# Performance work log

Measured on AMD Instinct MI355X. Metric: run time of the kernel, lower is better.

Reference implementation:

```python
import jax, jax.numpy as jnp
import numpy as np

B1, B2, CHUNK, HID, T = 64, 16, 128, 64, 131072
N_CHUNKS = 128


def setup_inputs() -> dict:
    key = jax.random.key(0)
    ks = jax.random.split(key, 12)
    # positive prices so log(p) is finite
    p = jax.random.uniform(ks[0], (T, 2), jnp.float32) * 2.0 + 0.5
    inds = jax.random.randint(ks[1], (B1,), 0, 100000, dtype=jnp.int32)
    open_slices = jax.random.randint(ks[2], (B1, B2, 1), 0, T, dtype=jnp.int32)
    ls_probs = jax.random.uniform(ks[3], (B1, B2, 1, 1), jnp.float32)
    open_probs = jax.random.uniform(ks[4], (B1, B2, 1, 1), jnp.float32)
    open_hx = jax.random.normal(ks[5], (B1, B2, 2, HID), jnp.float32) * 0.1
    s = 1.0 / np.sqrt(HID)
    # torch nn.LSTM params: gate order i,f,g,o
    W_ih = jax.random.uniform(ks[6], (4 * HID, 2), jnp.float32, -s, s)
    W_hh = jax.random.uniform(ks[7], (4 * HID, HID), jnp.float32, -s, s)
    b_ih = jax.random.uniform(ks[8], (4 * HID,), jnp.float32, -s, s)
    b_hh = jax.random.uniform(ks[9], (4 * HID,), jnp.float32, -s, s)
    W_out = jax.random.uniform(ks[10], (1, HID), jnp.float32, -s, s)
    b_out = jax.random.uniform(ks[11], (1,), jnp.float32, -s, s)
    return {"inds": inds, "p": p, "ls_probs": ls_probs, "open_probs": open_probs,
            "open_slices": open_slices, "open_hx": open_hx,
            "W_ih": W_ih, "W_hh": W_hh, "b_ih": b_ih, "b_hh": b_hh,
            "W_out": W_out, "b_out": b_out, "n_chunks": N_CHUNKS}


def reference(inds, p, ls_probs, open_probs, open_slices, open_hx,
              W_ih, W_hh, b_ih, b_hh, W_out, b_out, n_chunks):
    b1, b2 = open_hx.shape[:2]
    hid = open_hx.shape[-1]
    C = CHUNK
    h0 = open_hx[:, :, 0, :].reshape(b1 * b2, hid)
    c0 = open_hx[:, :, 1, :].reshape(b1 * b2, hid)
    open_logp = jnp.log(p[open_slices])  # (b1, b2, 1, 2)
    # sliding-window gather base: idx[i,j,t] = inds[i] + j + t (per-chunk offset added in scan)
    base = (inds[:, None, None]
            + jnp.arange(b2, dtype=inds.dtype)[None, :, None]
            + jnp.arange(C, dtype=inds.dtype)[None, None, :])  # (b1, b2, C)
    bias = b_ih + b_hh

    def lstm_chunk(x, h, c):  # x: (N, C, 2)
        xg = x @ W_ih.T + bias  # precompute input projection: (N, C, 4H)
        def step(carry, xg_t):
            h, c = carry
            g = xg_t + h @ W_hh.T
            i, f, gg, o = jnp.split(g, 4, axis=-1)
            c = jax.nn.sigmoid(f) * c + jax.nn.sigmoid(i) * jnp.tanh(gg)
            h = jax.nn.sigmoid(o) * jnp.tanh(c)
            return (h, c), h
        (h, c), hs = jax.lax.scan(step, (h, c), xg.swapaxes(0, 1))
        return hs.swapaxes(0, 1), h, c  # (N, C, H)

    def chunk_step(carry, offset):
        h, c, last_nd, loss = carry
        idx = base + offset * C                      # (b1, b2, C)
        p_chunk = p[idx]                             # (b1, b2, C, 2)
        x = p_chunk - p_chunk[:, :, :1, :]           # re-center on first step of chunk
        out, h, c = lstm_chunk(x.reshape(b1 * b2, C, 2), h, c)
        probs = jax.nn.sigmoid(out.reshape(b1, b2, C, hid) @ W_out.T + b_out)  # (b1,b2,C,1)
        not_done = last_nd * jnp.cumprod(1.0 - probs[:, :, :-1], axis=2)       # (b1,b2,C-1,1)
        probs = jnp.concatenate([probs[:, :, :1], probs[:, :, 1:] * not_done], axis=2)
        last_nd = not_done[:, :, -1:, :]
        logp = jnp.log(p_chunk)
        payoff = ls_probs * (logp - open_logp) + (1.0 - ls_probs) * (open_logp - logp)
        loss = loss + jnp.sum(open_probs * probs * payoff)
        return (h, c, last_nd, loss), None

    init = (h0, c0, jnp.ones((b1, b2, 1, 1), p.dtype), jnp.zeros((), p.dtype))
    (_, _, _, loss), _ = jax.lax.scan(chunk_step, init, jnp.arange(n_chunks))
    return loss
```

## Files before the change

### kernel.cpp

```cpp
#include <hip/hip_runtime.h>


#define CH  128
#define HID 64

typedef __fp16 f16x2 __attribute__((ext_vector_type(2)));

__device__ __forceinline__ float rlf(float v, int l) {
  return __builtin_bit_cast(float, __builtin_amdgcn_readlane(__builtin_bit_cast(int, v), l));
}
__device__ __forceinline__ int rli(int v, int l) { return __builtin_amdgcn_readlane(v, l); }
__device__ __forceinline__ int packh(float a, float b) {
  return __builtin_bit_cast(int, __builtin_amdgcn_cvt_pkrtz(a, b));
}
__device__ __forceinline__ f16x2 h2(int v) { return __builtin_bit_cast(f16x2, v); }
__device__ __forceinline__ float frcp(float x) { return __builtin_amdgcn_rcpf(x); }
__device__ __forceinline__ float sigm(float x) { return frcp(1.0f + __expf(-x)); }
__device__ __forceinline__ float tanh_(float x) {
  float e = __expf(2.0f * x);
  return 1.0f - 2.0f * frcp(e + 1.0f);
}
template <int CTRL, int RMASK>
__device__ __forceinline__ float dpp_add(float v) {
  int x = __builtin_amdgcn_update_dpp(0, __builtin_bit_cast(int, v), CTRL, RMASK, 0xF, true);
  return v + __builtin_bit_cast(float, x);
}
__device__ __forceinline__ float dpp_xor1(float v) {
  int x = __builtin_amdgcn_update_dpp(0, __builtin_bit_cast(int, v), 0xB1, 0xF, 0xF, true);
  return __builtin_bit_cast(float, x);
}
__device__ __forceinline__ float dpp_wave_sum(float v) {
  v = dpp_add<0x111, 0xF>(v);
  v = dpp_add<0x112, 0xF>(v);
  v = dpp_add<0x114, 0xF>(v);
  v = dpp_add<0x118, 0xF>(v);
  v = dpp_add<0x142, 0xA>(v);
  v = dpp_add<0x143, 0xC>(v);
  return v;
}

__global__ __attribute__((amdgpu_flat_work_group_size(128, 128), amdgpu_waves_per_eu(2, 2)))
void pc_lstm_kernel(const int* __restrict__ inds,
                    const float* __restrict__ p,
                    const float* __restrict__ ls_probs,
                    const float* __restrict__ open_probs,
                    const int* __restrict__ open_slices,
                    const float* __restrict__ open_hx,
                    const float* __restrict__ W_ih,
                    const float* __restrict__ W_hh,
                    const float* __restrict__ b_ih,
                    const float* __restrict__ b_hh,
                    const float* __restrict__ W_out,
                    const float* __restrict__ b_out,
                    const int* __restrict__ n_chunks_p,
                    float* __restrict__ out)
{
  __shared__ __fp16 ring[2][CH][HID];
  __shared__ int prod;
  __shared__ int cons;

  const int tid  = threadIdx.x;
  const int wv   = tid >> 6;
  const int lane = tid & 63;
  const int s    = blockIdx.x;
  const int n_chunks = n_chunks_p[0];
  const int tbase = inds[s >> 4] + (s & 15);
  const float2* p2 = (const float2*)p;

  if (tid == 0) { prod = 0; cons = 0; }
  __syncthreads();

  if (wv == 0) {
    int W0[HID / 2], W1[HID / 2], W2[HID / 2], W3[HID / 2];
    {
      const float2* r0 = (const float2*)(W_hh + (0 * HID + lane) * HID);
      const float2* r1 = (const float2*)(W_hh + (1 * HID + lane) * HID);
      const float2* r2 = (const float2*)(W_hh + (2 * HID + lane) * HID);
      const float2* r3 = (const float2*)(W_hh + (3 * HID + lane) * HID);
#pragma unroll
      for (int j = 0; j < HID / 2; ++j) {
        float2 v0 = r0[j], v1 = r1[j], v2 = r2[j], v3 = r3[j];
        W0[j] = packh(v0.x, v0.y);
        W1[j] = packh(v1.x, v1.y);
        W2[j] = packh(v2.x, v2.y);
        W3[j] = packh(v3.x, v3.y);
      }
    }
    float wxa[4], wxb[4], bb[4];
#pragma unroll
    for (int g = 0; g < 4; ++g) {
      const int r = g * HID + lane;
      wxa[g] = W_ih[2 * r];
      wxb[g] = W_ih[2 * r + 1];
      bb[g]  = b_ih[r] + b_hh[r];
    }
    float h = open_hx[(s * 2 + 0) * HID + lane];
    float c = open_hx[(s * 2 + 1) * HID + lane];

    float2 curA = p2[tbase + lane];
    float2 curB = p2[tbase + HID + lane];
    float2 nxtA = curA, nxtB = curB;

    for (int off = 0; off < n_chunks; ++off) {
      if (off) { curA = nxtA; curB = nxtB; }
      const float px0 = rlf(curA.x, 0);
      const float px1 = rlf(curA.y, 0);
      float2 xA, xB;
      xA.x = curA.x - px0; xA.y = curA.y - px1;
      xB.x = curB.x - px0; xB.y = curB.y - px1;
      if (off + 1 < n_chunks) {
        const int nb = tbase + (off + 1) * CH;
        nxtA = p2[nb + lane];
        nxtB = p2[nb + HID + lane];
      }
      while (__hip_atomic_load(&cons, __ATOMIC_ACQUIRE, __HIP_MEMORY_SCOPE_WORKGROUP) + 2 <= off)
        __builtin_amdgcn_s_sleep(8);

      __fp16* slot = &ring[off & 1][0][0];
#pragma unroll
      for (int hf = 0; hf < 2; ++hf) {
        const float xcx = hf ? xB.x : xA.x;
        const float xcy = hf ? xB.y : xA.y;
#pragma unroll 1
        for (int tl = 0; tl < 64; ++tl) {
          const int hp = packh(h, dpp_xor1(h));
          const float x0 = rlf(xcx, tl);
          const float x1 = rlf(xcy, tl);

          float A0 = bb[0], A1 = bb[1], A2 = bb[2], A3 = bb[3];
          float B0 = fmaf(x1, wxb[0], x0 * wxa[0]);
          float B1 = fmaf(x1, wxb[1], x0 * wxa[1]);
          float B2 = fmaf(x1, wxb[2], x0 * wxa[2]);
          float B3 = fmaf(x1, wxb[3], x0 * wxa[3]);
#pragma unroll
          for (int j = 0; j < 16; ++j) {
            const f16x2 ha = h2(rli(hp, 2 * j));
            const f16x2 hb = h2(rli(hp, 2 * j + 32));
            A0 = __builtin_amdgcn_fdot2(ha, h2(W0[j]),      A0, false);
            B0 = __builtin_amdgcn_fdot2(hb, h2(W0[j + 16]), B0, false);
            A1 = __builtin_amdgcn_fdot2(ha, h2(W1[j]),      A1, false);
            B1 = __builtin_amdgcn_fdot2(hb, h2(W1[j + 16]), B1, false);
            A2 = __builtin_amdgcn_fdot2(ha, h2(W2[j]),      A2, false);
            B2 = __builtin_amdgcn_fdot2(hb, h2(W2[j + 16]), B2, false);
            A3 = __builtin_amdgcn_fdot2(ha, h2(W3[j]),      A3, false);
            B3 = __builtin_amdgcn_fdot2(hb, h2(W3[j + 16]), B3, false);
          }
          const float ig = sigm(A0 + B0);
          const float fg = sigm(A1 + B1);
          const float gg = tanh_(A2 + B2);
          const float og = sigm(A3 + B3);
          c = fmaf(fg, c, ig * gg);
          h = og * tanh_(c);

          slot[(hf * 64 + tl) * HID + lane] = (__fp16)h;
        }
      }
      if (lane == 0)
        __hip_atomic_store(&prod, off + 1, __ATOMIC_RELEASE, __HIP_MEMORY_SCOPE_WORKGROUP);
    }
  } else {
    const float wo   = W_out[lane];
    const float bout = b_out[0];
    const int   os   = open_slices[s];
    const float OL   = __logf(p[2 * os]) + __logf(p[2 * os + 1]);
    const float coef = open_probs[s] * (2.0f * ls_probs[s] - 1.0f);

    float S = 1.0f, D = 1.0f, lsum = 0.0f, psum = 0.0f;

    for (int off = 0; off < n_chunks; ++off) {
      const int cb = tbase + off * CH;
      const float2 cA = p2[cb + lane];
      const float2 cB = p2[cb + HID + lane];
      const float LA = __logf(cA.x) + __logf(cA.y);
      const float LB = __logf(cB.x) + __logf(cB.y);

      while (__hip_atomic_load(&prod, __ATOMIC_ACQUIRE, __HIP_MEMORY_SCOPE_WORKGROUP) <= off)
        __builtin_amdgcn_s_sleep(32);

      const __fp16* slot = &ring[off & 1][0][0];
#pragma unroll 1
      for (int tt = 0; tt < CH; ++tt) {
        const float hv = (float)slot[tt * HID + lane];
        const float z  = rlf(dpp_wave_sum(hv * wo), 63);
        const float pr = sigm(z + bout);
        const float Lt = (tt < 64) ? rlf(LA, tt) : rlf(LB, tt - 64);
        const float pn = (tt == 0) ? pr : pr * D;
        lsum = fmaf(pn, Lt, lsum);
        psum += pn;
        if (tt == 0)           D = S * (1.0f - pr);
        else if (tt < CH - 1)  D *= (1.0f - pr);
        else                   S = D;
      }
      if (lane == 0)
        __hip_atomic_store(&cons, off + 1, __ATOMIC_RELEASE, __HIP_MEMORY_SCOPE_WORKGROUP);
    }
    if (lane == 0) atomicAdd(out, coef * (lsum - OL * psum));
  }
}

extern "C" void kernel_launch(void* const* d_in, const int* in_sizes, int n_in,
                              void* d_out, int out_size, void* d_ws, size_t ws_size,
                              hipStream_t stream) {
  (void)hipMemsetAsync(d_out, 0, sizeof(float), stream);

  pc_lstm_kernel<<<dim3(1024), dim3(128), 0, stream>>>(
      (const int*)d_in[0],
      (const float*)d_in[1],
      (const float*)d_in[2],
      (const float*)d_in[3],
      (const int*)d_in[4],
      (const float*)d_in[5],
      (const float*)d_in[6],
      (const float*)d_in[7],
      (const float*)d_in[8],
      (const float*)d_in[9],
      (const float*)d_in[10],
      (const float*)d_in[11],
      (const int*)d_in[12],
      (float*)d_out);
}
```

Baseline: 8.087 ms.

## Split recurrent matvec across both waves with per-step barrier handoff

Both waves now hold half of W_hh in registers. Wave 1 computes the partial dot product for the second half of h and passes it to wave 0 through LDS, in lockstep with two __syncthreads per timestep. This is meant to halve the serial fdot2 and readlane chain on the critical path. The loss computation on wave 1 is delayed by one chunk and interleaved into the same loop, replacing the atomic producer/consumer flags, and the waves_per_eu attribute is swapped for plain launch bounds. The cost is barrier and LDS round-trip latency added to every recurrent step.

```diff
diff --git a/kernel.cpp b/kernel.cpp
--- a/kernel.cpp
+++ b/kernel.cpp
@@ -39,7 +39,7 @@
   return v;
 }
 
-__global__ __attribute__((amdgpu_flat_work_group_size(128, 128), amdgpu_waves_per_eu(2, 2)))
+__global__ __launch_bounds__(128)
 void pc_lstm_kernel(const int* __restrict__ inds,
                     const float* __restrict__ p,
                     const float* __restrict__ ls_probs,
@@ -56,8 +56,8 @@
                     float* __restrict__ out)
 {
   __shared__ __fp16 ring[2][CH][HID];
-  __shared__ int prod;
-  __shared__ int cons;
+  __shared__ int    hpbuf[16];
+  __shared__ float  pbuf[64][4];
 
   const int tid  = threadIdx.x;
   const int wv   = tid >> 6;
@@ -67,26 +67,33 @@
   const int tbase = inds[s >> 4] + (s & 15);
   const float2* p2 = (const float2*)p;
 
-  if (tid == 0) { prod = 0; cons = 0; }
-  __syncthreads();
+  int W0[16], W1[16], W2[16], W3[16];
+  {
+    const int kb = wv * 32;
+    const float2* r0 = (const float2*)(W_hh + (0 * HID + lane) * HID + kb);
+    const float2* r1 = (const float2*)(W_hh + (1 * HID + lane) * HID + kb);
+    const float2* r2 = (const float2*)(W_hh + (2 * HID + lane) * HID + kb);
+    const float2* r3 = (const float2*)(W_hh + (3 * HID + lane) * HID + kb);
+#pragma unroll
+    for (int j = 0; j < 16; ++j) {
+      float2 v0 = r0[j], v1 = r1[j], v2 = r2[j], v3 = r3[j];
+      W0[j] = packh(v0.x, v0.y);
+      W1[j] = packh(v1.x, v1.y);
+      W2[j] = packh(v2.x, v2.y);
+      W3[j] = packh(v3.x, v3.y);
+    }
+  }
+
+  float wxa[4], wxb[4], bb[4];
+  float h = 0.0f, c = 0.0f;
+  int   hp = 0;
+  float2 nxtA, nxtB, xA, xB;
+  float wo = 0.0f, bout = 0.0f, OL = 0.0f, coef = 0.0f;
+  float S = 1.0f, D = 1.0f, lsum = 0.0f, psum = 0.0f;
+  float2 lagA, lagB;
+  float lagLA = 0.0f, lagLB = 0.0f;
 
   if (wv == 0) {
-    int W0[HID / 2], W1[HID / 2], W2[HID / 2], W3[HID / 2];
-    {
-      const float2* r0 = (const float2*)(W_hh + (0 * HID + lane) * HID);
-      const float2* r1 = (const float2*)(W_hh + (1 * HID + lane) * HID);
-      const float2* r2 = (const float2*)(W_hh + (2 * HID + lane) * HID);
-      const float2* r3 = (const float2*)(W_hh + (3 * HID + lane) * HID);
-#pragma unroll
-      for (int j = 0; j < HID / 2; ++j) {
-        float2 v0 = r0[j], v1 = r1[j], v2 = r2[j], v3 = r3[j];
-        W0[j] = packh(v0.x, v0.y);
-        W1[j] = packh(v1.x, v1.y);
-        W2[j] = packh(v2.x, v2.y);
-        W3[j] = packh(v3.x, v3.y);
-      }
-    }
-    float wxa[4], wxb[4], bb[4];
 #pragma unroll
     for (int g = 0; g < 4; ++g) {
       const int r = g * HID + lane;
@@ -94,18 +101,26 @@
       wxb[g] = W_ih[2 * r + 1];
       bb[g]  = b_ih[r] + b_hh[r];
     }
-    float h = open_hx[(s * 2 + 0) * HID + lane];
-    float c = open_hx[(s * 2 + 1) * HID + lane];
-
-    float2 curA = p2[tbase + lane];
-    float2 curB = p2[tbase + HID + lane];
-    float2 nxtA = curA, nxtB = curB;
-
-    for (int off = 0; off < n_chunks; ++off) {
-      if (off) { curA = nxtA; curB = nxtB; }
+    h = open_hx[(s * 2 + 0) * HID + lane];
+    c = open_hx[(s * 2 + 1) * HID + lane];
+    hp = packh(h, dpp_xor1(h));
+    if (lane >= 32 && !(lane & 1)) hpbuf[(lane - 32) >> 1] = hp;
+    nxtA = p2[tbase + lane];
+    nxtB = p2[tbase + HID + lane];
+  } else {
+    wo   = W_out[lane];
+    bout = b_out[0];
+    const int os = open_slices[s];
+    OL   = __logf(p[2 * os]) + __logf(p[2 * os + 1]);
+    coef = open_probs[s] * (2.0f * ls_probs[s] - 1.0f);
+  }
+  __syncthreads();
+
+  for (int off = 0; off < n_chunks; ++off) {
+    if (wv == 0) {
+      const float2 curA = nxtA, curB = nxtB;
       const float px0 = rlf(curA.x, 0);
       const float px1 = rlf(curA.y, 0);
-      float2 xA, xB;
       xA.x = curA.x - px0; xA.y = curA.y - px1;
       xB.x = curB.x - px0; xB.y = curB.y - px1;
       if (off + 1 < n_chunks) {
@@ -113,86 +128,102 @@
         nxtA = p2[nb + lane];
         nxtB = p2[nb + HID + lane];
       }
-      while (__hip_atomic_load(&cons, __ATOMIC_ACQUIRE, __HIP_MEMORY_SCOPE_WORKGROUP) + 2 <= off)
-        __builtin_amdgcn_s_sleep(8);
-
-      __fp16* slot = &ring[off & 1][0][0];
-#pragma unroll
-      for (int hf = 0; hf < 2; ++hf) {
-        const float xcx = hf ? xB.x : xA.x;
-        const float xcy = hf ? xB.y : xA.y;
+    } else {
+      if (off) {
+        lagLA = __logf(lagA.x) + __logf(lagA.y);
+        lagLB = __logf(lagB.x) + __logf(lagB.y);
+      }
+      const int lb = tbase + off * CH;
+      lagA = p2[lb + lane];
+      lagB = p2[lb + HID + lane];
+    }
+    const int doloss = (off > 0);
+    const int rpar = off & 1;
+
+#pragma unroll
+    for (int hf = 0; hf < 2; ++hf) {
 #pragma unroll 1
-        for (int tl = 0; tl < 64; ++tl) {
-          const int hp = packh(h, dpp_xor1(h));
-          const float x0 = rlf(xcx, tl);
-          const float x1 = rlf(xcy, tl);
-
-          float A0 = bb[0], A1 = bb[1], A2 = bb[2], A3 = bb[3];
-          float B0 = fmaf(x1, wxb[0], x0 * wxa[0]);
-          float B1 = fmaf(x1, wxb[1], x0 * wxa[1]);
-          float B2 = fmaf(x1, wxb[2], x0 * wxa[2]);
-          float B3 = fmaf(x1, wxb[3], x0 * wxa[3]);
+      for (int tl = 0; tl < 64; ++tl) {
+        const int tt = (hf << 6) + tl;
+        float A0, A1, A2, A3;
+        float hv = 0.0f;
+
+        if (wv == 0) {
+          const float x0 = rlf(hf ? xB.x : xA.x, tl);
+          const float x1 = rlf(hf ? xB.y : xA.y, tl);
+          A0 = fmaf(x1, wxb[0], fmaf(x0, wxa[0], bb[0]));
+          A1 = fmaf(x1, wxb[1], fmaf(x0, wxa[1], bb[1]));
+          A2 = fmaf(x1, wxb[2], fmaf(x0, wxa[2], bb[2]));
+          A3 = fmaf(x1, wxb[3], fmaf(x0, wxa[3], bb[3]));
 #pragma unroll
           for (int j = 0; j < 16; ++j) {
             const f16x2 ha = h2(rli(hp, 2 * j));
-            const f16x2 hb = h2(rli(hp, 2 * j + 32));
-            A0 = __builtin_amdgcn_fdot2(ha, h2(W0[j]),      A0, false);
-            B0 = __builtin_amdgcn_fdot2(hb, h2(W0[j + 16]), B0, false);
-            A1 = __builtin_amdgcn_fdot2(ha, h2(W1[j]),      A1, false);
-            B1 = __builtin_amdgcn_fdot2(hb, h2(W1[j + 16]), B1, false);
-            A2 = __builtin_amdgcn_fdot2(ha, h2(W2[j]),      A2, false);
-            B2 = __builtin_amdgcn_fdot2(hb, h2(W2[j + 16]), B2, false);
-            A3 = __builtin_amdgcn_fdot2(ha, h2(W3[j]),      A3, false);
-            B3 = __builtin_amdgcn_fdot2(hb, h2(W3[j + 16]), B3, false);
+            A0 = __builtin_amdgcn_fdot2(ha, h2(W0[j]), A0, false);
+            A1 = __builtin_amdgcn_fdot2(ha, h2(W1[j]), A1, false);
+            A2 = __builtin_amdgcn_fdot2(ha, h2(W2[j]), A2, false);
+            A3 = __builtin_amdgcn_fdot2(ha, h2(W3[j]), A3, false);
           }
-          const float ig = sigm(A0 + B0);
-          const float fg = sigm(A1 + B1);
-          const float gg = tanh_(A2 + B2);
-          const float og = sigm(A3 + B3);
+        } else {
+          const int hw = hpbuf[lane & 15];
+          if (doloss) hv = (float)ring[rpar ^ 1][tt][lane];
+          float P0 = 0.f, P1 = 0.f, P2 = 0.f, P3 = 0.f;
+#pragma unroll
+          for (int j = 0; j < 16; ++j) {
+            const f16x2 hb = h2(rli(hw, j));
+            P0 = __builtin_amdgcn_fdot2(hb, h2(W0[j]), P0, false);
+            P1 = __builtin_amdgcn_fdot2(hb, h2(W1[j]), P1, false);
+            P2 = __builtin_amdgcn_fdot2(hb, h2(W2[j]), P2, false);
+            P3 = __builtin_amdgcn_fdot2(hb, h2(W3[j]), P3, false);
+          }
+          pbuf[lane][0] = P0; pbuf[lane][1] = P1;
+          pbuf[lane][2] = P2; pbuf[lane][3] = P3;
+          A0 = A1 = A2 = A3 = 0.0f;
+        }
+        __syncthreads();
+
+        if (wv == 0) {
+          const float4 P = *(const float4*)&pbuf[lane][0];
+          const float ig = sigm(A0 + P.x);
+          const float fg = sigm(A1 + P.y);
+          const float gg = tanh_(A2 + P.z);
+          const float og = sigm(A3 + P.w);
           c = fmaf(fg, c, ig * gg);
           h = og * tanh_(c);
-
-          slot[(hf * 64 + tl) * HID + lane] = (__fp16)h;
+          hp = packh(h, dpp_xor1(h));
+          if (lane >= 32 && !(lane & 1)) hpbuf[(lane - 32) >> 1] = hp;
+          ring[rpar][tt][lane] = (__fp16)h;
+        } else if (doloss) {
+          const float z  = rlf(dpp_wave_sum(hv * wo), 63);
+          const float pr = sigm(z + bout);
+          const float Lt = hf ? rlf(lagLB, tl) : rlf(lagLA, tl);
+          const float pn = (tt == 0) ? pr : pr * D;
+          lsum = fmaf(pn, Lt, lsum);
+          psum += pn;
+          if (tt == 0)           D = S * (1.0f - pr);
+          else if (tt < CH - 1)  D *= (1.0f - pr);
+          else                   S = D;
         }
+        __syncthreads();
       }
-      if (lane == 0)
-        __hip_atomic_store(&prod, off + 1, __ATOMIC_RELEASE, __HIP_MEMORY_SCOPE_WORKGROUP);
-    }
-  } else {
-    const float wo   = W_out[lane];
-    const float bout = b_out[0];
-    const int   os   = open_slices[s];
-    const float OL   = __logf(p[2 * os]) + __logf(p[2 * os + 1]);
-    const float coef = open_probs[s] * (2.0f * ls_probs[s] - 1.0f);
-
-    float S = 1.0f, D = 1.0f, lsum = 0.0f, psum = 0.0f;
-
-    for (int off = 0; off < n_chunks; ++off) {
-      const int cb = tbase + off * CH;
-      const float2 cA = p2[cb + lane];
-      const float2 cB = p2[cb + HID + lane];
-      const float LA = __logf(cA.x) + __logf(cA.y);
-      const float LB = __logf(cB.x) + __logf(cB.y);
-
-      while (__hip_atomic_load(&prod, __ATOMIC_ACQUIRE, __HIP_MEMORY_SCOPE_WORKGROUP) <= off)
-        __builtin_amdgcn_s_sleep(32);
-
-      const __fp16* slot = &ring[off & 1][0][0];
+    }
+  }
+
+  if (wv == 1) {
+    lagLA = __logf(lagA.x) + __logf(lagA.y);
+    lagLB = __logf(lagB.x) + __logf(lagB.y);
+    const int rpar = (n_chunks - 1) & 1;
 #pragma unroll 1
-      for (int tt = 0; tt < CH; ++tt) {
-        const float hv = (float)slot[tt * HID + lane];
-        const float z  = rlf(dpp_wave_sum(hv * wo), 63);
-        const float pr = sigm(z + bout);
-        const float Lt = (tt < 64) ? rlf(LA, tt) : rlf(LB, tt - 64);
-        const float pn = (tt == 0) ? pr : pr * D;
-        lsum = fmaf(pn, Lt, lsum);
-        psum += pn;
-        if (tt == 0)           D = S * (1.0f - pr);
-        else if (tt < CH - 1)  D *= (1.0f - pr);
-        else                   S = D;
-      }
-      if (lane == 0)
-        __hip_atomic_store(&cons, off + 1, __ATOMIC_RELEASE, __HIP_MEMORY_SCOPE_WORKGROUP);
+    for (int tt = 0; tt < CH; ++tt) {
+      const float hv = (float)ring[rpar][tt][lane];
+      const float z  = rlf(dpp_wave_sum(hv * wo), 63);
+      const float pr = sigm(z + bout);
+      const float Lt = (tt < 64) ? rlf(lagLA, tt) : rlf(lagLB, tt - 64);
+      const float pn = (tt == 0) ? pr : pr * D;
+      lsum = fmaf(pn, Lt, lsum);
+      psum += pn;
+      if (tt == 0)           D = S * (1.0f - pr);
+      else if (tt < CH - 1)  D *= (1.0f - pr);
+      else                   S = D;
     }
     if (lane == 0) atomicAdd(out, coef * (lsum - OL * psum));
   }
```

Result: slower. 10.72 ms (+32.5%).

## Stream packed fp16 W_hh from global memory each step instead of holding it in registers

Applied to the files above, without the earlier changes.

Adds a staging kernel that packs W_hh into fp16 pairs laid out as int4 per lane and gate. The recurrent loop now loads these weights from global memory (L1/L2 cached) on every timestep instead of keeping 128 VGPRs of weights resident. This frees registers, but it puts 32 vector memory loads per step on the serial critical path of the LSTM recurrence, and their latency may dominate.

```diff
diff --git a/kernel.cpp b/kernel.cpp
--- a/kernel.cpp
+++ b/kernel.cpp
@@ -39,6 +39,18 @@
   return v;
 }
 
+__global__ void stage_w(const float* __restrict__ W_hh, int4* __restrict__ ws) {
+  const int lane = threadIdx.x;
+  const int j    = blockIdx.x;
+  const int k    = 2 * j;
+  int4 v;
+  v.x = packh(W_hh[(0 * HID + lane) * HID + k], W_hh[(0 * HID + lane) * HID + k + 1]);
+  v.y = packh(W_hh[(1 * HID + lane) * HID + k], W_hh[(1 * HID + lane) * HID + k + 1]);
+  v.z = packh(W_hh[(2 * HID + lane) * HID + k], W_hh[(2 * HID + lane) * HID + k + 1]);
+  v.w = packh(W_hh[(3 * HID + lane) * HID + k], W_hh[(3 * HID + lane) * HID + k + 1]);
+  ws[j * 64 + lane] = v;
+}
+
 __global__ __attribute__((amdgpu_flat_work_group_size(128, 128), amdgpu_waves_per_eu(2, 2)))
 void pc_lstm_kernel(const int* __restrict__ inds,
                     const float* __restrict__ p,
@@ -47,12 +59,12 @@
                     const int* __restrict__ open_slices,
                     const float* __restrict__ open_hx,
                     const float* __restrict__ W_ih,
-                    const float* __restrict__ W_hh,
                     const float* __restrict__ b_ih,
                     const float* __restrict__ b_hh,
                     const float* __restrict__ W_out,
                     const float* __restrict__ b_out,
                     const int* __restrict__ n_chunks_p,
+                    const int4* __restrict__ wpack,
                     float* __restrict__ out)
 {
   __shared__ __fp16 ring[2][CH][HID];
@@ -71,21 +83,6 @@
   __syncthreads();
 
   if (wv == 0) {
-    int W0[HID / 2], W1[HID / 2], W2[HID / 2], W3[HID / 2];
-    {
-      const float2* r0 = (const float2*)(W_hh + (0 * HID + lane) * HID);
-      const float2* r1 = (const float2*)(W_hh + (1 * HID + lane) * HID);
-      const float2* r2 = (const float2*)(W_hh + (2 * HID + lane) * HID);
-      const float2* r3 = (const float2*)(W_hh + (3 * HID + lane) * HID);
-#pragma unroll
-      for (int j = 0; j < HID / 2; ++j) {
-        float2 v0 = r0[j], v1 = r1[j], v2 = r2[j], v3 = r3[j];
-        W0[j] = packh(v0.x, v0.y);
-        W1[j] = packh(v1.x, v1.y);
-        W2[j] = packh(v2.x, v2.y);
-        W3[j] = packh(v3.x, v3.y);
-      }
-    }
     float wxa[4], wxb[4], bb[4];
 #pragma unroll
     for (int g = 0; g < 4; ++g) {
@@ -100,6 +97,8 @@
     float2 curA = p2[tbase + lane];
     float2 curB = p2[tbase + HID + lane];
     float2 nxtA = curA, nxtB = curB;
+
+    int woff = lane * (int)sizeof(int4);
 
     for (int off = 0; off < n_chunks; ++off) {
       if (off) { curA = nxtA; curB = nxtB; }
@@ -123,6 +122,9 @@
         const float xcy = hf ? xB.y : xA.y;
 #pragma unroll 1
         for (int tl = 0; tl < 64; ++tl) {
+          asm volatile("" : "+v"(woff));
+          const int4* wp = (const int4*)((const char*)wpack + woff);
+
           const int hp = packh(h, dpp_xor1(h));
           const float x0 = rlf(xcx, tl);
           const float x1 = rlf(xcy, tl);
@@ -134,16 +136,18 @@
           float B3 = fmaf(x1, wxb[3], x0 * wxa[3]);
 #pragma unroll
           for (int j = 0; j < 16; ++j) {
+            const int4 wa = wp[j * 64];
+            const int4 wb = wp[(j + 16) * 64];
             const f16x2 ha = h2(rli(hp, 2 * j));
             const f16x2 hb = h2(rli(hp, 2 * j + 32));
-            A0 = __builtin_amdgcn_fdot2(ha, h2(W0[j]),      A0, false);
-            B0 = __builtin_amdgcn_fdot2(hb, h2(W0[j + 16]), B0, false);
-            A1 = __builtin_amdgcn_fdot2(ha, h2(W1[j]),      A1, false);
-            B1 = __builtin_amdgcn_fdot2(hb, h2(W1[j + 16]), B1, false);
-            A2 = __builtin_amdgcn_fdot2(ha, h2(W2[j]),      A2, false);
-            B2 = __builtin_amdgcn_fdot2(hb, h2(W2[j + 16]), B2, false);
-            A3 = __builtin_amdgcn_fdot2(ha, h2(W3[j]),      A3, false);
-            B3 = __builtin_amdgcn_fdot2(hb, h2(W3[j + 16]), B3, false);
+            A0 = __builtin_amdgcn_fdot2(ha, h2(wa.x), A0, false);
+            B0 = __builtin_amdgcn_fdot2(hb, h2(wb.x), B0, false);
+            A1 = __builtin_amdgcn_fdot2(ha, h2(wa.y), A1, false);
+            B1 = __builtin_amdgcn_fdot2(hb, h2(wb.y), B1, false);
+            A2 = __builtin_amdgcn_fdot2(ha, h2(wa.z), A2, false);
+            B2 = __builtin_amdgcn_fdot2(hb, h2(wb.z), B2, false);
+            A3 = __builtin_amdgcn_fdot2(ha, h2(wa.w), A3, false);
+            B3 = __builtin_amdgcn_fdot2(hb, h2(wb.w), B3, false);
           }
           const float ig = sigm(A0 + B0);
           const float fg = sigm(A1 + B1);
@@ -203,6 +207,8 @@
                               hipStream_t stream) {
   (void)hipMemsetAsync(d_out, 0, sizeof(float), stream);
 
+  stage_w<<<dim3(32), dim3(64), 0, stream>>>((const float*)d_in[7], (int4*)d_ws);
+
   pc_lstm_kernel<<<dim3(1024), dim3(128), 0, stream>>>(
       (const int*)d_in[0],
       (const float*)d_in[1],
@@ -211,11 +217,11 @@
       (const int*)d_in[4],
       (const float*)d_in[5],
       (const float*)d_in[6],
-      (const float*)d_in[7],
       (const float*)d_in[8],
       (const float*)d_in[9],
       (const float*)d_in[10],
       (const float*)d_in[11],
       (const int*)d_in[12],
+      (const int4*)d_ws,
       (float*)d_out);
 }
```

New measurement: 18.66 ms. 131% more time.

## Compute LSTM recurrent matvec with MFMA 16x16x32 instead of fdot2 readlane loop

Applied to the files above, without the earlier changes.

Replaces the per-lane fdot2 loop, which broadcast h via 32 readlanes per step, with 32 MFMA 16x16x32 f16 ops per timestep. W_hh is held in registers as B fragments. h is spread into A fragments through ds_bpermute, and only row 0 of each output tile is used. The matvec wastes most of the MFMA rows, and each step now pays for ds_bpermute round-trips and MFMA latency on the serial recurrence. Launch bounds also change from the fixed waves_per_eu hint to __launch_bounds__(128).

```diff
diff --git a/kernel.cpp b/kernel.cpp
--- a/kernel.cpp
+++ b/kernel.cpp
@@ -4,16 +4,25 @@
 #define CH  128
 #define HID 64
 
-typedef __fp16 f16x2 __attribute__((ext_vector_type(2)));
+typedef __fp16 f16x8 __attribute__((ext_vector_type(8)));
+typedef float  f32x4 __attribute__((ext_vector_type(4)));
+typedef int    i32x4 __attribute__((ext_vector_type(4)));
+
+#define MFMA16(a, b, c) __builtin_amdgcn_mfma_f32_16x16x32_f16((a), (b), (c), 0, 0, 0)
 
 __device__ __forceinline__ float rlf(float v, int l) {
   return __builtin_bit_cast(float, __builtin_amdgcn_readlane(__builtin_bit_cast(int, v), l));
 }
-__device__ __forceinline__ int rli(int v, int l) { return __builtin_amdgcn_readlane(v, l); }
 __device__ __forceinline__ int packh(float a, float b) {
   return __builtin_bit_cast(int, __builtin_amdgcn_cvt_pkrtz(a, b));
 }
-__device__ __forceinline__ f16x2 h2(int v) { return __builtin_bit_cast(f16x2, v); }
+__device__ __forceinline__ int bperm(int byteaddr, int src) {
+  return __builtin_amdgcn_ds_bpermute(byteaddr, src);
+}
+__device__ __forceinline__ float bpermf(int byteaddr, float src) {
+  return __builtin_bit_cast(float,
+      __builtin_amdgcn_ds_bpermute(byteaddr, __builtin_bit_cast(int, src)));
+}
 __device__ __forceinline__ float frcp(float x) { return __builtin_amdgcn_rcpf(x); }
 __device__ __forceinline__ float sigm(float x) { return frcp(1.0f + __expf(-x)); }
 __device__ __forceinline__ float tanh_(float x) {
@@ -39,7 +48,7 @@
   return v;
 }
 
-__global__ __attribute__((amdgpu_flat_work_group_size(128, 128), amdgpu_waves_per_eu(2, 2)))
+__global__ __launch_bounds__(128)
 void pc_lstm_kernel(const int* __restrict__ inds,
                     const float* __restrict__ p,
                     const float* __restrict__ ls_probs,
@@ -71,21 +80,23 @@
   __syncthreads();
 
   if (wv == 0) {
-    int W0[HID / 2], W1[HID / 2], W2[HID / 2], W3[HID / 2];
-    {
-      const float2* r0 = (const float2*)(W_hh + (0 * HID + lane) * HID);
-      const float2* r1 = (const float2*)(W_hh + (1 * HID + lane) * HID);
-      const float2* r2 = (const float2*)(W_hh + (2 * HID + lane) * HID);
-      const float2* r3 = (const float2*)(W_hh + (3 * HID + lane) * HID);
-#pragma unroll
-      for (int j = 0; j < HID / 2; ++j) {
-        float2 v0 = r0[j], v1 = r1[j], v2 = r2[j], v3 = r3[j];
-        W0[j] = packh(v0.x, v0.y);
-        W1[j] = packh(v1.x, v1.y);
-        W2[j] = packh(v2.x, v2.y);
-        W3[j] = packh(v3.x, v3.y);
-      }
-    }
+    const int q  = lane >> 4;
+    const int lm = lane & 15;
+
+    f16x8 Bf[4][4][2];
+#pragma unroll
+    for (int g = 0; g < 4; ++g)
+#pragma unroll
+      for (int cb = 0; cb < 4; ++cb)
+#pragma unroll
+        for (int kh = 0; kh < 2; ++kh) {
+          const float* src = W_hh + (g * HID + 16 * cb + lm) * HID + 32 * kh + 8 * q;
+          f16x8 b;
+#pragma unroll
+          for (int j = 0; j < 8; ++j) b[j] = (__fp16)src[j];
+          Bf[g][cb][kh] = b;
+        }
+
     float wxa[4], wxb[4], bb[4];
 #pragma unroll
     for (int g = 0; g < 4; ++g) {
@@ -96,6 +107,14 @@
     }
     float h = open_hx[(s * 2 + 0) * HID + lane];
     float c = open_hx[(s * 2 + 1) * HID + lane];
+
+    int aadr0[4], aadr1[4];
+#pragma unroll
+    for (int m = 0; m < 4; ++m) {
+      aadr0[m] = 8 * (4 * q + m);
+      aadr1[m] = 8 * (16 + 4 * q + m);
+    }
+    const int dadr = 4 * lm;
 
     float2 curA = p2[tbase + lane];
     float2 curB = p2[tbase + HID + lane];
@@ -124,31 +143,49 @@
 #pragma unroll 1
         for (int tl = 0; tl < 64; ++tl) {
           const int hp = packh(h, dpp_xor1(h));
+          i32x4 t0, t1;
+#pragma unroll
+          for (int m = 0; m < 4; ++m) {
+            t0[m] = bperm(aadr0[m], hp);
+            t1[m] = bperm(aadr1[m], hp);
+          }
+          const f16x8 a0 = __builtin_bit_cast(f16x8, t0);
+          const f16x8 a1 = __builtin_bit_cast(f16x8, t1);
+
+          const f32x4 z4 = {0.0f, 0.0f, 0.0f, 0.0f};
+          f32x4 C[4][4];
+#pragma unroll
+          for (int g = 0; g < 4; ++g)
+#pragma unroll
+            for (int cb = 0; cb < 4; ++cb) {
+              f32x4 acc = MFMA16(a0, Bf[g][cb][0], z4);
+              C[g][cb] = MFMA16(a1, Bf[g][cb][1], acc);
+            }
+
           const float x0 = rlf(xcx, tl);
           const float x1 = rlf(xcy, tl);
-
-          float A0 = bb[0], A1 = bb[1], A2 = bb[2], A3 = bb[3];
-          float B0 = fmaf(x1, wxb[0], x0 * wxa[0]);
-          float B1 = fmaf(x1, wxb[1], x0 * wxa[1]);
-          float B2 = fmaf(x1, wxb[2], x0 * wxa[2]);
-          float B3 = fmaf(x1, wxb[3], x0 * wxa[3]);
-#pragma unroll
-          for (int j = 0; j < 16; ++j) {
-            const f16x2 ha = h2(rli(hp, 2 * j));
-            const f16x2 hb = h2(rli(hp, 2 * j + 32));
-            A0 = __builtin_amdgcn_fdot2(ha, h2(W0[j]),      A0, false);
-            B0 = __builtin_amdgcn_fdot2(hb, h2(W0[j + 16]), B0, false);
-            A1 = __builtin_amdgcn_fdot2(ha, h2(W1[j]),      A1, false);
-            B1 = __builtin_amdgcn_fdot2(hb, h2(W1[j + 16]), B1, false);
-            A2 = __builtin_amdgcn_fdot2(ha, h2(W2[j]),      A2, false);
-            B2 = __builtin_amdgcn_fdot2(hb, h2(W2[j + 16]), B2, false);
-            A3 = __builtin_amdgcn_fdot2(ha, h2(W3[j]),      A3, false);
-            B3 = __builtin_amdgcn_fdot2(hb, h2(W3[j + 16]), B3, false);
-          }
-          const float ig = sigm(A0 + B0);
-          const float fg = sigm(A1 + B1);
-          const float gg = tanh_(A2 + B2);
-          const float og = sigm(A3 + B3);
+          float xg[4];
+#pragma unroll
+          for (int g = 0; g < 4; ++g)
+            xg[g] = fmaf(x1, wxb[g], fmaf(x0, wxa[g], bb[g]));
+
+          float r[4][4];
+#pragma unroll
+          for (int g = 0; g < 4; ++g)
+#pragma unroll
+            for (int cb = 0; cb < 4; ++cb)
+              r[g][cb] = bpermf(dadr, C[g][cb][0]);
+
+          float pre[4];
+#pragma unroll
+          for (int g = 0; g < 4; ++g)
+            pre[g] = ((q == 0) ? r[g][0] : (q == 1) ? r[g][1]
+                    : (q == 2) ? r[g][2] : r[g][3]) + xg[g];
+
+          const float ig = sigm(pre[0]);
+          const float fg = sigm(pre[1]);
+          const float gg = tanh_(pre[2]);
+          const float og = sigm(pre[3]);
           c = fmaf(fg, c, ig * gg);
           h = og * tanh_(c);
 
```

New measurement: 15.01 ms. 1.86x slower.
